# Kernel optimization log

Hardware: AMD Instinct MI355X
Metric: run time of the kernel (lower is better)

Reference implementation:

```python
import jax, jax.numpy as jnp
import numpy as np

HEADS = 20
HEAD_DIM = 64
NUM_IP = 20          # num_content_tokens (4) + num_style_tokens (16)
FU_SCALE = 0.5
STYLE_SCALE = 1.0
SCALE = 1.0 / np.sqrt(HEAD_DIM).astype(np.float32)


def setup_inputs() -> dict:
    key = jax.random.key(0)
    ks = jax.random.split(key, 9)
    B, S, H, C = 4, 4096, 1280, 2048
    T = 77 + NUM_IP  # text tokens + ip tokens
    w = 0.02
    return {
        "hidden_states": jax.random.normal(ks[0], (B, S, H), jnp.float32),
        "encoder_hidden_states": jax.random.normal(ks[1], (B, T, C), jnp.float32),
        "Wq": jax.random.normal(ks[2], (H, H), jnp.float32) * w,
        "Wk": jax.random.normal(ks[3], (H, C), jnp.float32) * w,
        "Wv": jax.random.normal(ks[4], (H, C), jnp.float32) * w,
        "Wk_ip": jax.random.normal(ks[5], (H, C), jnp.float32) * w,
        "Wv_ip": jax.random.normal(ks[6], (H, C), jnp.float32) * w,
        "Wo": jax.random.normal(ks[7], (H, H), jnp.float32) * w,
        "bo": jnp.zeros((H,), jnp.float32),
    }


def _to_heads(x):
    # [B, T, H] -> [B, heads, T, head_dim]
    B, T, _ = x.shape
    return x.reshape(B, T, HEADS, HEAD_DIM).transpose(0, 2, 1, 3)


def _blend(p):
    # cross-batch prob fusion: rows 1<-0, 3<-2 (CFG pairs)
    p = p.at[1].set(FU_SCALE * p[1] + (1.0 - FU_SCALE) * p[0])
    p = p.at[3].set(FU_SCALE * p[3] + (1.0 - FU_SCALE) * p[2])
    return p


def reference(hidden_states, encoder_hidden_states, Wq, Wk, Wv, Wk_ip, Wv_ip, Wo, bo):
    B, S, H = hidden_states.shape
    text = encoder_hidden_states[:, :-NUM_IP, :]   # [B, 77, C]
    ip = encoder_hidden_states[:, -NUM_IP:, :]     # [B, 20, C]

    q = _to_heads(hidden_states @ Wq.T)            # [B, h, S, d]
    k = _to_heads(text @ Wk.T)                     # [B, h, 77, d]
    v = _to_heads(text @ Wv.T)

    # fuAttn branch: explicit probs, blended across batch, then PV matmul
    probs = jax.nn.softmax(jnp.einsum('bhqd,bhkd->bhqk', q, k) * SCALE, axis=-1)
    probs = _blend(probs)
    raw = jnp.einsum('bhqk,bhkd->bhqd', probs, v)
    raw = raw.transpose(0, 2, 1, 3).reshape(B, S, H)

    # IP-adapter style cross-attention (fuIPAttn branch)
    ip_k = _to_heads(ip @ Wk_ip.T)                 # [B, h, 20, d]
    ip_v = _to_heads(ip @ Wv_ip.T)
    ip_probs = jax.nn.softmax(jnp.einsum('bhqd,bhkd->bhqk', q, ip_k) * SCALE, axis=-1)
    ip_probs = _blend(ip_probs)
    ip_hs = jnp.einsum('bhqk,bhkd->bhqd', ip_probs, ip_v)
    ip_hs = ip_hs.transpose(0, 2, 1, 3).reshape(B, S, H)

    hs = raw + STYLE_SCALE * ip_hs
    # batch rows 0 and 2 keep raw (text-only) attention output
    hs = hs.at[0].set(raw[0]).at[2].set(raw[2])

    # to_out[0] linear (bias) + to_out[1] dropout (identity at inference)
    return hs @ Wo.T + bo
```

## Files before the change

### kernel.cpp

```cpp
#include <hip/hip_runtime.h>
#include <cstdint>

typedef float floatx4 __attribute__((ext_vector_type(4)));
typedef __bf16 bf16x8 __attribute__((ext_vector_type(8)));

typedef const __attribute__((address_space(1))) void* gas_cvp;
typedef __attribute__((address_space(3))) void* las_vp;

__device__ __forceinline__ float bflo(unsigned int u) {
    return __builtin_bit_cast(float, u << 16);
}
__device__ __forceinline__ float bfhi(unsigned int u) {
    return __builtin_bit_cast(float, u & 0xffff0000u);
}
__device__ __forceinline__ unsigned short f2bf(float f) {
    unsigned int u = __builtin_bit_cast(unsigned int, f);
    u += 0x7fffu + ((u >> 16) & 1u);
    return (unsigned short)(u >> 16);
}
__device__ __forceinline__ bf16x8 ld8(const unsigned short* p) {
    return __builtin_bit_cast(bf16x8, *(const uint4*)p);
}
__device__ __forceinline__ floatx4 mfma32(bf16x8 a, bf16x8 b, floatx4 c) {
    return __builtin_amdgcn_mfma_f32_16x16x32_bf16(a, b, c, 0, 0, 0);
}
__device__ __forceinline__ void load_lds16(const void* g, void* l) {
    __builtin_amdgcn_global_load_lds(
        (gas_cvp)(unsigned long long)g,
        (las_vp)(unsigned int)(unsigned long long)l,
        16, 0, 0);
}

__global__ void cvt_f32_bf16(const float* __restrict__ in,
                             unsigned short* __restrict__ out, int n4) {
    int i = blockIdx.x * 256 + threadIdx.x;
    if (i < n4) {
        float4 v = ((const float4*)in)[i];
        ushort4 o;
        o.x = f2bf(v.x); o.y = f2bf(v.y); o.z = f2bf(v.z); o.w = f2bf(v.w);
        ((ushort4*)out)[i] = o;
    }
}

struct CvtJob { const float* src; unsigned short* dst; int n4; };
struct CvtJobs { CvtJob j[6]; };

__global__ void cvt_multi(CvtJobs jobs) {
    CvtJob jb = jobs.j[blockIdx.y];
    int i = blockIdx.x * 256 + threadIdx.x;
    if (i < jb.n4) {
        float4 v = ((const float4*)jb.src)[i];
        ushort4 o;
        o.x = f2bf(v.x); o.y = f2bf(v.y); o.z = f2bf(v.z); o.w = f2bf(v.w);
        ((ushort4*)jb.dst)[i] = o;
    }
}

__global__ void cvt_ehs(const float* __restrict__ ehs,
                        unsigned short* __restrict__ text,
                        unsigned short* __restrict__ ip) {
    int i = blockIdx.x * 256 + threadIdx.x;
    if (i < 384 * 512) {
        int r = i >> 9, c = i & 511;
        int b = r / 96, t = r - b * 96;
        ushort4 o = {0, 0, 0, 0};
        if (t < 77) {
            float4 v = *(const float4*)&ehs[((size_t)(b * 97 + t)) * 2048 + c * 4];
            o.x = f2bf(v.x); o.y = f2bf(v.y); o.z = f2bf(v.z); o.w = f2bf(v.w);
        }
        ((ushort4*)text)[i] = o;
    } else {
        int i2 = i - 384 * 512;
        if (i2 < 128 * 512) {
            int r = i2 >> 9, c = i2 & 511;
            int b = r >> 5, t = r & 31;
            ushort4 o = {0, 0, 0, 0};
            if (t < 20) {
                float4 v = *(const float4*)&ehs[((size_t)(b * 97 + 77 + t)) * 2048 + c * 4];
                o.x = f2bf(v.x); o.y = f2bf(v.y); o.z = f2bf(v.z); o.w = f2bf(v.w);
            }
            ((ushort4*)ip)[i2] = o;
        }
    }
}

struct GJob {
    const unsigned short* A;
    const unsigned short* B;
    void* C;
    int M, K;
    int Bn;
    int nt;
    int ldc;
    int bstart;
};
struct GArgs { GJob j[5]; };

#define GBAR() do { __builtin_amdgcn_s_barrier(); __builtin_amdgcn_sched_barrier(0); } while (0)

template <bool F32OUT>
__global__ __launch_bounds__(512, 2) void gemm256(GArgs args,
                                                  const float* __restrict__ bias) {
    const int tid = threadIdx.x;
    int jid = 0;
#pragma unroll
    for (int t = 1; t < 5; ++t)
        if ((int)blockIdx.x >= args.j[t].bstart) jid = t;
    const GJob jb = args.j[jid];
    const int K = jb.K;
    int b = (int)blockIdx.x - jb.bstart;
    {
        const int mt = (jb.M + 255) >> 8;
        const int nblk = mt * jb.nt;
        if ((nblk & 7) == 0) b = (b & 7) * (nblk >> 3) + (b >> 3);
    }
    const int by = b / jb.nt, bx = b - by * jb.nt;

    __shared__ unsigned short ldsA[32768];
    __shared__ unsigned short ldsB[32768];

    const int srow   = ((tid >> 7) << 4) + ((tid >> 2) & 15);
    const int schunk = ((tid & 3) << 4) ^ (((tid >> 2) & 6) << 3);
    const int scol   = (((tid >> 6) & 1) << 5) + (schunk >> 1);

    const int Mloc = jb.M, BnL = jb.Bn;

    const unsigned short* pA[2][2];
    const unsigned short* pB[2][2];
    unsigned short* dA[2][2];
    unsigned short* dB[2][2];
#pragma unroll
    for (int h = 0; h < 2; ++h)
#pragma unroll
        for (int j = 0; j < 2; ++j) {
            const int r = h * 128 + j * 64 + srow;
            int ra = by * 256 + r;  ra = (ra < Mloc) ? ra : (Mloc - 1);
            int rb2 = bx * 256 + r; rb2 = (rb2 < BnL) ? rb2 : (BnL - 1);
            pA[h][j] = jb.A + (size_t)ra * K + scol;
            pB[h][j] = jb.B + (size_t)rb2 * K + scol;
            dA[h][j] = &ldsA[h * 8192 + j * 4096 + tid * 8];
            dB[h][j] = &ldsB[h * 8192 + j * 4096 + tid * 8];
        }

    const int lane = tid & 63, fr = lane & 15, g = lane >> 4;
    const int w = tid >> 6, wr = w & 1, wc = w >> 1;
    const int rb   = fr * 32 + ((g * 8) ^ ((fr & 6) << 2));
    const int aoff = wr * 8192 + rb;
    const int boff = (wc >> 1) * 8192 + (wc & 1) * 4096 + rb;

    floatx4 acc[8][4] = {};
    bf16x8 af[4][2], bn0[2][2], bn1[2][2];

    const int KT = K >> 6;

    load_lds16(pA[0][0], dA[0][0]); load_lds16(pA[0][1], dA[0][1]);
    load_lds16(pA[1][0], dA[1][0]); load_lds16(pA[1][1], dA[1][1]);
    load_lds16(pB[0][0], dB[0][0]); load_lds16(pB[0][1], dB[0][1]);
    load_lds16(pB[1][0], dB[1][0]); load_lds16(pB[1][1], dB[1][1]);
    load_lds16(pB[0][0] + 64, dB[0][0] + 16384);
    load_lds16(pB[0][1] + 64, dB[0][1] + 16384);
    load_lds16(pA[0][0] + 64, dA[0][0] + 16384);
    load_lds16(pA[0][1] + 64, dA[0][1] + 16384);
    asm volatile("s_waitcnt vmcnt(4)" ::: "memory");
    GBAR();

    for (int u = 0; u < KT; ++u) {
        const int pb = (u & 1) << 14;
        const int qb = pb ^ 16384;
        const int k1 = (u + 1 < KT) ? (u + 1) : (KT - 1);
        const int k2 = (u + 2 < KT) ? (u + 2) : (KT - 1);

#pragma unroll
        for (int mi = 0; mi < 4; ++mi)
#pragma unroll
            for (int kk = 0; kk < 2; ++kk)
                af[mi][kk] = *(const bf16x8*)&ldsA[pb + aoff + (mi * 2 + kk) * 512];
#pragma unroll
        for (int nf = 0; nf < 2; ++nf)
#pragma unroll
            for (int kk = 0; kk < 2; ++kk)
                bn0[nf][kk] = *(const bf16x8*)&ldsB[pb + boff + (nf * 2 + kk) * 512];
        load_lds16(pA[1][0] + (size_t)k1 * 64, dA[1][0] + qb);
        load_lds16(pA[1][1] + (size_t)k1 * 64, dA[1][1] + qb);
        GBAR();
        __builtin_amdgcn_s_setprio(1);
#pragma unroll
        for (int kk = 0; kk < 2; ++kk)
#pragma unroll
            for (int mi = 0; mi < 4; ++mi)
#pragma unroll
                for (int nf = 0; nf < 2; ++nf)
                    acc[mi][nf] = mfma32(af[mi][kk], bn0[nf][kk], acc[mi][nf]);
        __builtin_amdgcn_s_setprio(0);
        GBAR();

#pragma unroll
        for (int nf = 0; nf < 2; ++nf)
#pragma unroll
            for (int kk = 0; kk < 2; ++kk)
                bn1[nf][kk] = *(const bf16x8*)&ldsB[pb + boff + ((nf + 2) * 2 + kk) * 512];
        load_lds16(pB[1][0] + (size_t)k1 * 64, dB[1][0] + qb);
        load_lds16(pB[1][1] + (size_t)k1 * 64, dB[1][1] + qb);
        GBAR();
        __builtin_amdgcn_s_setprio(1);
#pragma unroll
        for (int kk = 0; kk < 2; ++kk)
#pragma unroll
            for (int mi = 0; mi < 4; ++mi)
#pragma unroll
                for (int nf = 0; nf < 2; ++nf)
                    acc[mi][nf + 2] = mfma32(af[mi][kk], bn1[nf][kk], acc[mi][nf + 2]);
        __builtin_amdgcn_s_setprio(0);
        GBAR();

#pragma unroll
        for (int mi = 0; mi < 4; ++mi)
#pragma unroll
            for (int kk = 0; kk < 2; ++kk)
                af[mi][kk] = *(const bf16x8*)&ldsA[pb + aoff + ((mi + 4) * 2 + kk) * 512];
        load_lds16(pB[0][0] + (size_t)k2 * 64, dB[0][0] + pb);
        load_lds16(pB[0][1] + (size_t)k2 * 64, dB[0][1] + pb);
        GBAR();
        __builtin_amdgcn_s_setprio(1);
#pragma unroll
        for (int kk = 0; kk < 2; ++kk)
#pragma unroll
            for (int mi = 0; mi < 4; ++mi)
#pragma unroll
                for (int nf = 0; nf < 2; ++nf)
                    acc[mi + 4][nf + 2] = mfma32(af[mi][kk], bn1[nf][kk], acc[mi + 4][nf + 2]);
        __builtin_amdgcn_s_setprio(0);
        GBAR();

        load_lds16(pA[0][0] + (size_t)k2 * 64, dA[0][0] + pb);
        load_lds16(pA[0][1] + (size_t)k2 * 64, dA[0][1] + pb);
        GBAR();
        __builtin_amdgcn_s_setprio(1);
#pragma unroll
        for (int kk = 0; kk < 2; ++kk)
#pragma unroll
            for (int mi = 0; mi < 4; ++mi)
#pragma unroll
                for (int nf = 0; nf < 2; ++nf)
                    acc[mi + 4][nf] = mfma32(af[mi][kk], bn0[nf][kk], acc[mi + 4][nf]);
        __builtin_amdgcn_s_setprio(0);
        asm volatile("s_waitcnt vmcnt(4)" ::: "memory");
        GBAR();
    }
    asm volatile("s_waitcnt vmcnt(0)" ::: "memory");

    const int colBase = bx * 256 + wc * 64;
    const int rowBase = by * 256 + wr * 128;
    const int ldc = jb.ldc;
    float bv[4] = {};
    if (F32OUT) {
#pragma unroll
        for (int nf = 0; nf < 4; ++nf) bv[nf] = bias[colBase + nf * 16 + fr];
    }
#pragma unroll
    for (int mi = 0; mi < 8; ++mi) {
#pragma unroll
        for (int nf = 0; nf < 4; ++nf) {
            const int col  = colBase + nf * 16 + fr;
            const int row0 = rowBase + mi * 16 + g * 4;
#pragma unroll
            for (int r = 0; r < 4; ++r) {
                const int row = row0 + r;
                if (row < Mloc) {
                    float v = acc[mi][nf][r];
                    if (F32OUT)
                        ((float*)jb.C)[(size_t)row * ldc + col] = v + bv[nf];
                    else
                        ((unsigned short*)jb.C)[(size_t)row * ldc + col] = f2bf(v);
                }
            }
        }
    }
}

#define NT 77
#define NI 20

__global__ __launch_bounds__(256, 4) void attn_mfma(
    const unsigned short* __restrict__ q,
    const unsigned short* __restrict__ kt,
    const unsigned short* __restrict__ vtT,
    const unsigned short* __restrict__ kip,
    const unsigned short* __restrict__ ipT,
    unsigned short* __restrict__ outp)
{
    const int tid = threadIdx.x;
    const int qt = blockIdx.x;
    const int h  = blockIdx.y;
    const int pz = blockIdx.z;
    const int b0 = 2 * pz;
    const int lane  = tid & 63;
    const int w     = tid >> 6;
    const int bi    = w >> 1;
    const int strip = (w & 1) * 16;
    const int fr = lane & 15;
    const int g  = lane >> 4;

    __shared__ unsigned short sP[2][32][104];

    for (int i = tid; i < 2 * 32 * 24; i += 256) {
        int b = i / (32 * 24); int rem = i % (32 * 24);
        sP[b][rem / 24][80 + rem % 24] = 0;
    }

    const size_t qbase = ((size_t)((b0 + bi) * 4096 + qt * 32 + strip + fr)) * 1280 + h * 64;
    bf16x8 aq0 = ld8(&q[qbase + g * 8]);
    bf16x8 aq1 = ld8(&q[qbase + 32 + g * 8]);

    floatx4 sc[5] = {};
#pragma unroll
    for (int t = 0; t < 5; t++) {
        int key = t * 16 + fr;
        const size_t kb = ((size_t)((b0 + bi) * 96 + key)) * 1280 + h * 64;
        sc[t] = mfma32(aq0, ld8(&kt[kb + g * 8]), sc[t]);
        sc[t] = mfma32(aq1, ld8(&kt[kb + 32 + g * 8]), sc[t]);
    }

#pragma unroll
    for (int r = 0; r < 4; r++) {
        float m = -1e30f;
#pragma unroll
        for (int t = 0; t < 5; t++) {
            float v = sc[t][r] * 0.125f;
            if (t == 4 && fr >= 13) v = -1e30f;
            sc[t][r] = v;
            m = fmaxf(m, v);
        }
        m = fmaxf(m, __shfl_xor(m, 1));
        m = fmaxf(m, __shfl_xor(m, 2));
        m = fmaxf(m, __shfl_xor(m, 4));
        m = fmaxf(m, __shfl_xor(m, 8));
        float sum = 0.f;
#pragma unroll
        for (int t = 0; t < 5; t++) {
            float e = __expf(sc[t][r] - m);
            sc[t][r] = e;
            sum += e;
        }
        sum += __shfl_xor(sum, 1);
        sum += __shfl_xor(sum, 2);
        sum += __shfl_xor(sum, 4);
        sum += __shfl_xor(sum, 8);
        float inv = 1.f / sum;
#pragma unroll
        for (int t = 0; t < 5; t++)
            sP[bi][strip + g * 4 + r][t * 16 + fr] = f2bf(sc[t][r] * inv);
    }
    __syncthreads();

    {
        unsigned int* p0 = (unsigned int*)&sP[0][0][0];
        unsigned int* p1 = (unsigned int*)&sP[1][0][0];
        for (int i = tid; i < 32 * 104 / 2; i += 256) {
            unsigned int a = p0[i], b = p1[i];
            unsigned short r0 = f2bf(0.5f * (bflo(a) + bflo(b)));
            unsigned short r1 = f2bf(0.5f * (bfhi(a) + bfhi(b)));
            p1[i] = (unsigned int)r0 | ((unsigned int)r1 << 16);
        }
    }
    __syncthreads();

    floatx4 accO[4] = {};
    {
        const unsigned short* prow = &sP[bi][strip + fr][0];
        bf16x8 pa0 = ld8(prow + g * 8);
        bf16x8 pa1 = ld8(prow + 32 + g * 8);
        bf16x8 pa2 = ld8(prow + 64 + g * 8);
        const int vcol = (b0 + bi) * 96;
#pragma unroll
        for (int dt = 0; dt < 4; dt++) {
            const unsigned short* vrow = &vtT[(size_t)(h * 64 + dt * 16 + fr) * 512 + vcol];
            accO[dt] = mfma32(pa0, ld8(vrow + g * 8), accO[dt]);
            accO[dt] = mfma32(pa1, ld8(vrow + 32 + g * 8), accO[dt]);
            accO[dt] = mfma32(pa2, ld8(vrow + 64 + g * 8), accO[dt]);
        }
    }

    floatx4 si[2] = {};
#pragma unroll
    for (int t = 0; t < 2; t++) {
        int key = t * 16 + fr;
        const size_t kb = ((size_t)((b0 + bi) * 32 + key)) * 1280 + h * 64;
        si[t] = mfma32(aq0, ld8(&kip[kb + g * 8]), si[t]);
        si[t] = mfma32(aq1, ld8(&kip[kb + 32 + g * 8]), si[t]);
    }
#pragma unroll
    for (int r = 0; r < 4; r++) {
        float v0 = si[0][r] * 0.125f;
        float v1 = (fr >= 4) ? -1e30f : si[1][r] * 0.125f;
        float m = fmaxf(v0, v1);
        m = fmaxf(m, __shfl_xor(m, 1));
        m = fmaxf(m, __shfl_xor(m, 2));
        m = fmaxf(m, __shfl_xor(m, 4));
        m = fmaxf(m, __shfl_xor(m, 8));
        float e0 = __expf(v0 - m), e1 = __expf(v1 - m);
        float s = e0 + e1;
        s += __shfl_xor(s, 1);
        s += __shfl_xor(s, 2);
        s += __shfl_xor(s, 4);
        s += __shfl_xor(s, 8);
        float inv = 1.f / s;
        si[0][r] = e0 * inv;
        si[1][r] = e1 * inv;
    }
    __syncthreads();

#pragma unroll
    for (int r = 0; r < 4; r++) {
        sP[bi][strip + g * 4 + r][fr]      = f2bf(si[0][r]);
        sP[bi][strip + g * 4 + r][16 + fr] = f2bf(si[1][r]);
    }
    __syncthreads();

    for (int i = tid; i < 32 * 16; i += 256) {
        int r = i >> 4, kk = i & 15;
        unsigned int* p0 = (unsigned int*)&sP[0][r][0];
        unsigned int* p1 = (unsigned int*)&sP[1][r][0];
        unsigned int a = p0[kk], b = p1[kk];
        unsigned short r0 = f2bf(0.5f * (bflo(a) + bflo(b)));
        unsigned short r1 = f2bf(0.5f * (bfhi(a) + bfhi(b)));
        p1[kk] = (unsigned int)r0 | ((unsigned int)r1 << 16);
    }
    __syncthreads();

    if (bi == 1) {
        const unsigned short* prow = &sP[1][strip + fr][0];
        bf16x8 pip = ld8(prow + g * 8);
        const int icol = (b0 + 1) * 32;
#pragma unroll
        for (int dt = 0; dt < 4; dt++)
            accO[dt] = mfma32(pip,
                              ld8(&ipT[(size_t)(h * 64 + dt * 16 + fr) * 256 + icol + g * 8]),
                              accO[dt]);
    }

    const size_t orow0 = (size_t)((b0 + bi) * 4096 + qt * 32 + strip);
#pragma unroll
    for (int dt = 0; dt < 4; dt++) {
        int col = h * 64 + dt * 16 + fr;
#pragma unroll
        for (int r = 0; r < 4; r++)
            outp[(orow0 + g * 4 + r) * 1280 + col] = f2bf(accO[dt][r]);
    }
}

extern "C" void kernel_launch(void* const* d_in, const int* in_sizes, int n_in,
                              void* d_out, int out_size, void* d_ws, size_t ws_size,
                              hipStream_t stream) {
    const float* hs   = (const float*)d_in[0];
    const float* ehs  = (const float*)d_in[1];
    const float* Wq   = (const float*)d_in[2];
    const float* Wk   = (const float*)d_in[3];
    const float* Wv   = (const float*)d_in[4];
    const float* Wkip = (const float*)d_in[5];
    const float* Wvip = (const float*)d_in[6];
    const float* Wo   = (const float*)d_in[7];
    const float* bo   = (const float*)d_in[8];

    char* w = (char*)d_ws;
    size_t off = 0;
    auto alloc = [&](size_t bytes) {
        char* pp = w + off;
        off += (bytes + 255) & ~(size_t)255;
        return pp;
    };
    unsigned short* hs_bf   = (unsigned short*)alloc(16384ull * 1280 * 2);
    unsigned short* q_bf    = (unsigned short*)alloc(16384ull * 1280 * 2);
    unsigned short* at_bf   = (unsigned short*)alloc(16384ull * 1280 * 2);
    unsigned short* text_pad= (unsigned short*)alloc(384ull * 2048 * 2);
    unsigned short* ip_pad  = (unsigned short*)alloc(128ull * 2048 * 2);
    unsigned short* Wq_bf   = (unsigned short*)alloc(1280ull * 1280 * 2);
    unsigned short* Wk_bf   = (unsigned short*)alloc(1280ull * 2048 * 2);
    unsigned short* Wv_bf   = (unsigned short*)alloc(1280ull * 2048 * 2);
    unsigned short* Wkip_bf = (unsigned short*)alloc(1280ull * 2048 * 2);
    unsigned short* Wvip_bf = (unsigned short*)alloc(1280ull * 2048 * 2);
    unsigned short* Wo_bf   = (unsigned short*)alloc(1280ull * 1280 * 2);
    unsigned short* kt  = (unsigned short*)alloc(384ull * 1280 * 2);
    unsigned short* vtT = (unsigned short*)alloc(1280ull * 512 * 2);
    unsigned short* kip = (unsigned short*)alloc(128ull * 1280 * 2);
    unsigned short* ipT = (unsigned short*)alloc(1280ull * 256 * 2);

    cvt_f32_bf16<<<dim3(20480, 1, 1), 256, 0, stream>>>(hs, hs_bf, 16384 * 1280 / 4);

    cvt_ehs<<<dim3(1024, 1, 1), 256, 0, stream>>>(ehs, text_pad, ip_pad);

    CvtJobs cj{};
    cj.j[0] = CvtJob{Wq,   Wq_bf,   1280 * 1280 / 4};
    cj.j[1] = CvtJob{Wk,   Wk_bf,   1280 * 2048 / 4};
    cj.j[2] = CvtJob{Wv,   Wv_bf,   1280 * 2048 / 4};
    cj.j[3] = CvtJob{Wkip, Wkip_bf, 1280 * 2048 / 4};
    cj.j[4] = CvtJob{Wvip, Wvip_bf, 1280 * 2048 / 4};
    cj.j[5] = CvtJob{Wo,   Wo_bf,   1280 * 1280 / 4};
    cvt_multi<<<dim3(2560, 6, 1), 256, 0, stream>>>(cj);

    GArgs g1{};
    g1.j[0] = GJob{text_pad, Wk_bf,   (void*)kt,    384, 2048, 1280, 5, 1280,  0};
    g1.j[1] = GJob{ip_pad,   Wkip_bf, (void*)kip,   128, 2048, 1280, 5, 1280, 10};
    g1.j[2] = GJob{Wv_bf,    text_pad,(void*)vtT,  1280, 2048,  384, 2,  512, 15};
    g1.j[3] = GJob{Wvip_bf,  ip_pad,  (void*)ipT,  1280, 2048,  128, 1,  256, 25};
    g1.j[4] = GJob{hs_bf,    Wq_bf,   (void*)q_bf,16384, 1280, 1280, 5, 1280, 30};
    gemm256<false><<<dim3(350, 1, 1), 512, 0, stream>>>(g1, nullptr);

    attn_mfma<<<dim3(128, 20, 2), 256, 0, stream>>>(q_bf, kt, vtT, kip, ipT, at_bf);

    GArgs g2{};
    g2.j[0] = GJob{at_bf, Wo_bf, d_out, 16384, 1280, 1280, 5, 1280, 0};
    for (int t = 1; t < 5; ++t) g2.j[t].bstart = 0x7fffffff;
    gemm256<true><<<dim3(320, 1, 1), 512, 0, stream>>>(g2, bo);
}
```

Measured before the change: 440.1 us.

## Replace ping-pong 4-phase GEMM main loop with simple double-buffered loop

The GEMM main loop drops its interleaved four-phase schedule, which had several barriers per K-step and a two-step-ahead prefetch. It now issues all next-tile global-to-LDS loads up front, computes the full 8x4 MFMA tile per 32-wide k slice, then waits on vmcnt(0) and uses a single barrier per iteration. This cuts barrier count and simplifies scheduling. In exchange, prefetch depth drops to one tile and waiting on all outstanding loads every iteration may expose memory latency. It also raises register pressure from holding 12 fragments at once.

Result: no change. 439.6 us (-0.1%).

```diff
diff --git a/kernel.cpp b/kernel.cpp
--- a/kernel.cpp
+++ b/kernel.cpp
@@ -96,8 +96,6 @@
 };
 struct GArgs { GJob j[5]; };
 
-#define GBAR() do { __builtin_amdgcn_s_barrier(); __builtin_amdgcn_sched_barrier(0); } while (0)
-
 template <bool F32OUT>
 __global__ __launch_bounds__(512, 2) void gemm256(GArgs args,
                                                   const float* __restrict__ bias) {
@@ -149,105 +147,54 @@
     const int boff = (wc >> 1) * 8192 + (wc & 1) * 4096 + rb;
 
     floatx4 acc[8][4] = {};
-    bf16x8 af[4][2], bn0[2][2], bn1[2][2];
 
     const int KT = K >> 6;
 
-    load_lds16(pA[0][0], dA[0][0]); load_lds16(pA[0][1], dA[0][1]);
-    load_lds16(pA[1][0], dA[1][0]); load_lds16(pA[1][1], dA[1][1]);
-    load_lds16(pB[0][0], dB[0][0]); load_lds16(pB[0][1], dB[0][1]);
-    load_lds16(pB[1][0], dB[1][0]); load_lds16(pB[1][1], dB[1][1]);
-    load_lds16(pB[0][0] + 64, dB[0][0] + 16384);
-    load_lds16(pB[0][1] + 64, dB[0][1] + 16384);
-    load_lds16(pA[0][0] + 64, dA[0][0] + 16384);
-    load_lds16(pA[0][1] + 64, dA[0][1] + 16384);
-    asm volatile("s_waitcnt vmcnt(4)" ::: "memory");
-    GBAR();
+#pragma unroll
+    for (int h = 0; h < 2; ++h)
+#pragma unroll
+        for (int j = 0; j < 2; ++j) {
+            load_lds16(pA[h][j], dA[h][j]);
+            load_lds16(pB[h][j], dB[h][j]);
+        }
+    asm volatile("s_waitcnt vmcnt(0)" ::: "memory");
+    __builtin_amdgcn_s_barrier();
 
     for (int u = 0; u < KT; ++u) {
         const int pb = (u & 1) << 14;
         const int qb = pb ^ 16384;
         const int k1 = (u + 1 < KT) ? (u + 1) : (KT - 1);
-        const int k2 = (u + 2 < KT) ? (u + 2) : (KT - 1);
-
-#pragma unroll
-        for (int mi = 0; mi < 4; ++mi)
-#pragma unroll
-            for (int kk = 0; kk < 2; ++kk)
-                af[mi][kk] = *(const bf16x8*)&ldsA[pb + aoff + (mi * 2 + kk) * 512];
-#pragma unroll
-        for (int nf = 0; nf < 2; ++nf)
-#pragma unroll
-            for (int kk = 0; kk < 2; ++kk)
-                bn0[nf][kk] = *(const bf16x8*)&ldsB[pb + boff + (nf * 2 + kk) * 512];
-        load_lds16(pA[1][0] + (size_t)k1 * 64, dA[1][0] + qb);
-        load_lds16(pA[1][1] + (size_t)k1 * 64, dA[1][1] + qb);
-        GBAR();
-        __builtin_amdgcn_s_setprio(1);
-#pragma unroll
-        for (int kk = 0; kk < 2; ++kk)
-#pragma unroll
-            for (int mi = 0; mi < 4; ++mi)
-#pragma unroll
-                for (int nf = 0; nf < 2; ++nf)
-                    acc[mi][nf] = mfma32(af[mi][kk], bn0[nf][kk], acc[mi][nf]);
-        __builtin_amdgcn_s_setprio(0);
-        GBAR();
-
-#pragma unroll
-        for (int nf = 0; nf < 2; ++nf)
-#pragma unroll
-            for (int kk = 0; kk < 2; ++kk)
-                bn1[nf][kk] = *(const bf16x8*)&ldsB[pb + boff + ((nf + 2) * 2 + kk) * 512];
-        load_lds16(pB[1][0] + (size_t)k1 * 64, dB[1][0] + qb);
-        load_lds16(pB[1][1] + (size_t)k1 * 64, dB[1][1] + qb);
-        GBAR();
-        __builtin_amdgcn_s_setprio(1);
-#pragma unroll
-        for (int kk = 0; kk < 2; ++kk)
-#pragma unroll
-            for (int mi = 0; mi < 4; ++mi)
-#pragma unroll
-                for (int nf = 0; nf < 2; ++nf)
-                    acc[mi][nf + 2] = mfma32(af[mi][kk], bn1[nf][kk], acc[mi][nf + 2]);
-        __builtin_amdgcn_s_setprio(0);
-        GBAR();
-
-#pragma unroll
-        for (int mi = 0; mi < 4; ++mi)
-#pragma unroll
-            for (int kk = 0; kk < 2; ++kk)
-                af[mi][kk] = *(const bf16x8*)&ldsA[pb + aoff + ((mi + 4) * 2 + kk) * 512];
-        load_lds16(pB[0][0] + (size_t)k2 * 64, dB[0][0] + pb);
-        load_lds16(pB[0][1] + (size_t)k2 * 64, dB[0][1] + pb);
-        GBAR();
-        __builtin_amdgcn_s_setprio(1);
-#pragma unroll
-        for (int kk = 0; kk < 2; ++kk)
-#pragma unroll
-            for (int mi = 0; mi < 4; ++mi)
-#pragma unroll
-                for (int nf = 0; nf < 2; ++nf)
-                    acc[mi + 4][nf + 2] = mfma32(af[mi][kk], bn1[nf][kk], acc[mi + 4][nf + 2]);
-        __builtin_amdgcn_s_setprio(0);
-        GBAR();
-
-        load_lds16(pA[0][0] + (size_t)k2 * 64, dA[0][0] + pb);
-        load_lds16(pA[0][1] + (size_t)k2 * 64, dA[0][1] + pb);
-        GBAR();
-        __builtin_amdgcn_s_setprio(1);
-#pragma unroll
-        for (int kk = 0; kk < 2; ++kk)
-#pragma unroll
-            for (int mi = 0; mi < 4; ++mi)
-#pragma unroll
-                for (int nf = 0; nf < 2; ++nf)
-                    acc[mi + 4][nf] = mfma32(af[mi][kk], bn0[nf][kk], acc[mi + 4][nf]);
-        __builtin_amdgcn_s_setprio(0);
-        asm volatile("s_waitcnt vmcnt(4)" ::: "memory");
-        GBAR();
-    }
-    asm volatile("s_waitcnt vmcnt(0)" ::: "memory");
+
+#pragma unroll
+        for (int h = 0; h < 2; ++h)
+#pragma unroll
+            for (int j = 0; j < 2; ++j) {
+                load_lds16(pA[h][j] + (size_t)k1 * 64, dA[h][j] + qb);
+                load_lds16(pB[h][j] + (size_t)k1 * 64, dB[h][j] + qb);
+            }
+        __builtin_amdgcn_sched_barrier(0);
+
+#pragma unroll
+        for (int kk = 0; kk < 2; ++kk) {
+            bf16x8 af[8], bfr[4];
+#pragma unroll
+            for (int mi = 0; mi < 8; ++mi)
+                af[mi] = *(const bf16x8*)&ldsA[pb + aoff + (mi * 2 + kk) * 512];
+#pragma unroll
+            for (int nf = 0; nf < 4; ++nf)
+                bfr[nf] = *(const bf16x8*)&ldsB[pb + boff + (nf * 2 + kk) * 512];
+            __builtin_amdgcn_s_setprio(1);
+#pragma unroll
+            for (int mi = 0; mi < 8; ++mi)
+#pragma unroll
+                for (int nf = 0; nf < 4; ++nf)
+                    acc[mi][nf] = mfma32(af[mi], bfr[nf], acc[mi][nf]);
+            __builtin_amdgcn_s_setprio(0);
+        }
+
+        asm volatile("s_waitcnt vmcnt(0)" ::: "memory");
+        __builtin_amdgcn_s_barrier();
+    }
 
     const int colBase = bx * 256 + wc * 64;
     const int rowBase = by * 256 + wr * 128;
```
